# Kernel optimization log

Measured on AMD Instinct MI355X. Metric: run time of the kernel, lower is better.

The kernel has to match this reference:

```python
import jax, jax.numpy as jnp
import numpy as np

FEAT = 64      # feature_dim
HEADS = 4      # n_head
LATENT = 256   # latent_dim
G = 128        # num graphs
NPG = 150      # nodes per graph (<=180 for one-hot positions)
N = G * NPG    # 19200 nodes
E = N * 12     # 230400 edges (excl. self loops)
POS = 180      # one-hot position classes
SLOPE = 0.2    # PyG GATConv leaky_relu negative slope


def gat_conv(x, src, dst, W, att_s, att_d, bias):
    """PyG GATConv (concat heads, self loops already appended to src/dst)."""
    n = x.shape[0]
    h = (x @ W).reshape(n, HEADS, FEAT)                 # [N,H,F]
    a_s = jnp.sum(h * att_s, axis=-1)                   # [N,H]
    a_d = jnp.sum(h * att_d, axis=-1)                   # [N,H]
    e = jax.nn.leaky_relu(a_s[src] + a_d[dst], SLOPE)   # [E,H] per-edge logits
    m = jax.ops.segment_max(e, dst, num_segments=n)     # segment softmax over dst
    ex = jnp.exp(e - m[dst])
    s = jax.ops.segment_sum(ex, dst, num_segments=n)
    alpha = ex / (s[dst] + 1e-16)
    out = jax.ops.segment_sum(h[src] * alpha[:, :, None], dst, num_segments=n)
    return out.reshape(n, HEADS * FEAT) + bias


def setup_inputs() -> dict:
    key = jax.random.key(0)
    ks = jax.random.split(key, 20)

    def p(k, shape, fan_in):
        return jax.random.normal(k, shape, jnp.float32) / np.sqrt(fan_in).astype(np.float32)

    z = jax.random.normal(ks[0], (G, LATENT), jnp.float32)
    src = jax.random.randint(ks[1], (E,), 0, N, jnp.int32)
    dst = (src + jax.random.randint(ks[2], (E,), 1, N, jnp.int32)) % N  # no self loops
    edge_index = jnp.stack([src, dst])
    batch = jnp.repeat(jnp.arange(G, dtype=jnp.int32), NPG)

    in1 = FEAT + POS
    in2 = FEAT * HEADS
    inp = dict(z=z, edge_index=edge_index, batch=batch, num_graphs=G)
    inp.update(
        W0=p(ks[3], (LATENT, FEAT), LATENT), b0=jnp.zeros(FEAT, jnp.float32),
        W1=p(ks[4], (in1, HEADS * FEAT), in1),
        as1=p(ks[5], (HEADS, FEAT), FEAT), ad1=p(ks[6], (HEADS, FEAT), FEAT),
        bb1=jnp.zeros(HEADS * FEAT, jnp.float32),
        W2=p(ks[7], (in2, HEADS * FEAT), in2),
        as2=p(ks[8], (HEADS, FEAT), FEAT), ad2=p(ks[9], (HEADS, FEAT), FEAT),
        bb2=jnp.zeros(HEADS * FEAT, jnp.float32),
        W3=p(ks[10], (in2, HEADS * FEAT), in2),
        as3=p(ks[11], (HEADS, FEAT), FEAT), ad3=p(ks[12], (HEADS, FEAT), FEAT),
        bb3=jnp.zeros(HEADS * FEAT, jnp.float32),
        Wg=p(ks[13], (in2, FEAT), in2), bg=jnp.zeros(FEAT, jnp.float32),
        Wf=p(ks[14], (FEAT, 5), FEAT), bf=jnp.zeros(5, jnp.float32),
    )
    return inp


def reference(z, edge_index, batch, num_graphs,
              W0, b0, W1, as1, ad1, bb1, W2, as2, ad2, bb2,
              W3, as3, ad3, bb3, Wg, bg, Wf, bf):
    n = batch.shape[0]
    x = z @ W0 + b0                                    # dec_feature_init
    x = x[batch]                                       # broadcast graph latent to nodes
    # node_order_within_batch (batch is sorted)
    counts = jax.ops.segment_sum(jnp.ones_like(batch), batch, num_segments=num_graphs)
    starts = jnp.cumsum(counts) - counts
    order = jnp.arange(n, dtype=batch.dtype) - starts[batch]
    pos = jax.nn.one_hot(order, POS, dtype=x.dtype)
    x = jax.nn.relu(jnp.concatenate([x, pos], axis=1))
    # GATConv adds self loops by default
    loops = jnp.arange(n, dtype=edge_index.dtype)
    src = jnp.concatenate([edge_index[0], loops])
    dst = jnp.concatenate([edge_index[1], loops])
    x = jax.nn.relu(gat_conv(x, src, dst, W1, as1, ad1, bb1))
    x = jax.nn.relu(gat_conv(x, src, dst, W2, as2, ad2, bb2))
    x = jax.nn.relu(gat_conv(x, src, dst, W3, as3, ad3, bb3))
    x = jax.nn.relu(x @ Wg + bg)                       # dec_geo
    return x @ Wf + bf                                 # fc_geo -> [N,5]
```

## Files before the change

### kernel.cpp

```cpp
#include <hip/hip_runtime.h>
#include <hip/hip_fp16.h>

#define GNUM 128
#define HEADS 4
#define FEAT 64
#define CH 256
#define LAT 256
#define SLOPE 0.2f
#define CAP 64
#define POSMAX 180

typedef _Float16 h16;
typedef __attribute__((ext_vector_type(4))) _Float16 half4;
typedef __attribute__((ext_vector_type(8))) _Float16 half8;
typedef __attribute__((ext_vector_type(4))) float floatx4;

__device__ __forceinline__ float lrelu(float x) { return fmaxf(x, SLOPE * x); }

__global__ __launch_bounds__(256) void k_setup(const int* __restrict__ batch, int* __restrict__ cnt,
                                               int* __restrict__ starts, int n,
                                               const float* __restrict__ W2, const float* __restrict__ W3,
                                               const float* __restrict__ Wg, h16* __restrict__ W2T,
                                               h16* __restrict__ W3T, h16* __restrict__ WgT,
                                               const float* __restrict__ z, const float* __restrict__ W0,
                                               const float* __restrict__ b0, const float* __restrict__ W1,
                                               const float* __restrict__ as1, const float* __restrict__ ad1,
                                               float* __restrict__ A, float* __restrict__ asg,
                                               float* __restrict__ adg, float* __restrict__ asp,
                                               float* __restrict__ adp) {
  __shared__ float red[4][FEAT];
  __shared__ float xzs[FEAT];
  int bx = blockIdx.x, t = threadIdx.x;
  if (bx < 576) {
    int idx = bx * 256 + t;
    if (idx < n) {
      cnt[idx] = 0;
      int b = batch[idx];
      if (idx == 0 || batch[idx - 1] != b) starts[b] = idx;
    }
    if (idx < 65536) {
      int kb = idx >> 13, rem = idx & 8191, j = rem >> 8, nn = rem & 255;
      W2T[kb * 8192 + nn * 32 + j] = (h16)W2[(kb * 32 + j) * 256 + nn];
    } else if (idx < 131072) {
      int l = idx - 65536;
      int kb = l >> 13, rem = l & 8191, j = rem >> 8, nn = rem & 255;
      W3T[kb * 8192 + nn * 32 + j] = (h16)W3[(kb * 32 + j) * 256 + nn];
    } else {
      int l = idx - 131072;
      int kb = l >> 11, rem = l & 2047, j = rem >> 6, nn = rem & 63;
      WgT[kb * 2048 + nn * 32 + j] = (h16)Wg[(kb * 32 + j) * 64 + nn];
    }
  } else if (bx < 576 + GNUM) {
    int g = bx - 576;
    int f = t & 63, kq = t >> 6;
    float acc = 0.f;
    for (int k = kq * 64; k < kq * 64 + 64; ++k) acc += z[g * LAT + k] * W0[k * FEAT + f];
    red[kq][f] = acc;
    __syncthreads();
    if (kq == 0)
      xzs[f] = fmaxf(red[0][f] + red[1][f] + red[2][f] + red[3][f] + b0[f], 0.f);
    __syncthreads();
    float a2 = 0.f;
#pragma unroll 16
    for (int k = 0; k < FEAT; ++k) a2 += xzs[k] * W1[k * CH + t];
    A[g * CH + t] = a2;
    float ps = a2 * as1[t], pd = a2 * ad1[t];
#pragma unroll
    for (int sh = 1; sh < 64; sh <<= 1) {
      ps += __shfl_xor(ps, sh, 64);
      pd += __shfl_xor(pd, sh, 64);
    }
    if ((t & 63) == 0) {
      asg[g * 4 + (t >> 6)] = ps;
      adg[g * 4 + (t >> 6)] = pd;
    }
  } else {
    int p = bx - (576 + GNUM);
    float wv = W1[(size_t)(FEAT + p) * CH + t];
    float ps = wv * as1[t], pd = wv * ad1[t];
#pragma unroll
    for (int sh = 1; sh < 64; sh <<= 1) {
      ps += __shfl_xor(ps, sh, 64);
      pd += __shfl_xor(pd, sh, 64);
    }
    if ((t & 63) == 0) {
      asp[p * 4 + (t >> 6)] = ps;
      adp[p * 4 + (t >> 6)] = pd;
    }
  }
}

__global__ __launch_bounds__(256) void k_pre(const float* __restrict__ A, const float* __restrict__ W1,
                                             const int* __restrict__ batch, const int* __restrict__ starts,
                                             const float* __restrict__ asg, const float* __restrict__ adg,
                                             const float* __restrict__ asp, const float* __restrict__ adp,
                                             h16* __restrict__ H16, float* __restrict__ a_s,
                                             float* __restrict__ a_d, int n,
                                             const int* __restrict__ src, const int* __restrict__ dst,
                                             int* __restrict__ cnt, int* __restrict__ bucket, int e,
                                             int h1blocks) {
  int t = threadIdx.x;
  if ((int)blockIdx.x < h1blocks) {
    int row = blockIdx.x * 8 + (t >> 5);
    if (row < n) {
      int g = batch[row];
      int p = row - starts[g];
      int c0 = (t & 31) * 8;
      const float* ap = A + g * CH + c0;
      const float* wp = W1 + (size_t)(FEAT + p) * CH + c0;
      float4 a0 = *(const float4*)ap;
      float4 a1 = *(const float4*)(ap + 4);
      float4 w0v = *(const float4*)wp;
      float4 w1v = *(const float4*)(wp + 4);
      half8 o;
      o[0] = (h16)(a0.x + w0v.x); o[1] = (h16)(a0.y + w0v.y);
      o[2] = (h16)(a0.z + w0v.z); o[3] = (h16)(a0.w + w0v.w);
      o[4] = (h16)(a1.x + w1v.x); o[5] = (h16)(a1.y + w1v.y);
      o[6] = (h16)(a1.z + w1v.z); o[7] = (h16)(a1.w + w1v.w);
      *(half8*)(H16 + (size_t)row * CH + c0) = o;
    }
    int idx = blockIdx.x * 256 + t;
    if (idx < n * 4) {
      int nn = idx >> 2, h = idx & 3;
      int g2 = batch[nn], p2 = nn - starts[g2];
      a_s[idx] = asg[g2 * 4 + h] + asp[p2 * 4 + h];
      a_d[idx] = adg[g2 * 4 + h] + adp[p2 * 4 + h];
    }
  } else {
    int i = (blockIdx.x - h1blocks) * 256 + t;
    if (i < e) {
      int d = dst[i];
      int p = atomicAdd(&cnt[d], 1);
      if (p < CAP) bucket[d * CAP + p] = src[i];
    }
  }
}

__global__ __launch_bounds__(1024) void k_fgg(const h16* __restrict__ H16i, const float* __restrict__ a_si,
                                              const float* __restrict__ a_di, const float* __restrict__ bias,
                                              const int* __restrict__ cnt, const int* __restrict__ bucket,
                                              const h16* __restrict__ WT, const float* __restrict__ att_s,
                                              const float* __restrict__ att_d, h16* __restrict__ H16o,
                                              float* __restrict__ a_so, float* __restrict__ a_do_) {
  __shared__ float wsh[16][CAP][4];
  __shared__ int bsh[16][CAP];
  __shared__ __align__(16) h16 Xs[16 * 264];
  __shared__ float pls[16][16];
  __shared__ float pld[16][16];
  int t = threadIdx.x, wv = t >> 6, lane = t & 63;
  int quad = lane >> 4, l15 = lane & 15;
  int row0 = blockIdx.x * 16;
  int n = row0 + wv;
  int hh = lane >> 4, fo = lane * 4;
  {
    int c = min(cnt[n], CAP);
    bool valid = lane < c;
    int sc = valid ? bucket[n * CAP + lane] : n;
    if (valid) bsh[wv][lane] = sc;
    float4 ea4 = *(const float4*)(a_si + (size_t)sc * 4);
    float4 sn4 = *(const float4*)(a_si + (size_t)n * 4);
    float4 dn4 = *(const float4*)(a_di + (size_t)n * 4);
    float ea[4] = {ea4.x, ea4.y, ea4.z, ea4.w};
    float sn[4] = {sn4.x, sn4.y, sn4.z, sn4.w};
    float dn[4] = {dn4.x, dn4.y, dn4.z, dn4.w};
    float asf[4];
#pragma unroll
    for (int h = 0; h < 4; ++h) {
      float e = valid ? lrelu(ea[h] + dn[h]) : -1e30f;
      float es = lrelu(sn[h] + dn[h]);
      float m = e;
#pragma unroll
      for (int sh = 1; sh < 64; sh <<= 1) m = fmaxf(m, __shfl_xor(m, sh, 64));
      m = fmaxf(m, es);
      float wgt = valid ? __expf(e - m) : 0.f;
      float ws = __expf(es - m);
      float s = wgt;
#pragma unroll
      for (int sh = 1; sh < 64; sh <<= 1) s += __shfl_xor(s, sh, 64);
      s += ws;
      float inv = 1.f / (s + 1e-16f);
      if (valid) wsh[wv][lane][h] = wgt * inv;
      asf[h] = ws * inv;
    }
    half4 hv = *(const half4*)(H16i + (size_t)n * CH + fo);
    float a_self = asf[hh];
    float acc0 = a_self * (float)hv[0];
    float acc1 = a_self * (float)hv[1];
    float acc2 = a_self * (float)hv[2];
    float acc3 = a_self * (float)hv[3];
#define GLD(k) (*(const half4*)(H16i + (size_t)bsh[wv][k] * CH + fo))
    half4 q0, q1, q2, q3, q4, q5, q6, q7;
    if (c > 0) q0 = GLD(0);
    if (c > 1) q1 = GLD(1);
    if (c > 2) q2 = GLD(2);
    if (c > 3) q3 = GLD(3);
    if (c > 4) q4 = GLD(4);
    if (c > 5) q5 = GLD(5);
    if (c > 6) q6 = GLD(6);
    if (c > 7) q7 = GLD(7);
    for (int j0 = 0; j0 < c; j0 += 8) {
#define STEP(K, QK)                                              \
      if (j0 + K < c) {                                          \
        float wj = wsh[wv][j0 + K][hh];                          \
        half4 hc = QK;                                           \
        if (j0 + K + 8 < c) QK = GLD(j0 + K + 8);                \
        acc0 += wj * (float)hc[0];                               \
        acc1 += wj * (float)hc[1];                               \
        acc2 += wj * (float)hc[2];                               \
        acc3 += wj * (float)hc[3];                               \
      }
      STEP(0, q0) STEP(1, q1) STEP(2, q2) STEP(3, q3)
      STEP(4, q4) STEP(5, q5) STEP(6, q6) STEP(7, q7)
#undef STEP
    }
#undef GLD
    float4 b4 = *(const float4*)(bias + fo);
    half4 o;
    o[0] = (h16)fmaxf(acc0 + b4.x, 0.f);
    o[1] = (h16)fmaxf(acc1 + b4.y, 0.f);
    o[2] = (h16)fmaxf(acc2 + b4.z, 0.f);
    o[3] = (h16)fmaxf(acc3 + b4.w, 0.f);
    *(half4*)&Xs[wv * 264 + fo] = o;
  }
  __syncthreads();
  floatx4 acc = (floatx4){0.f, 0.f, 0.f, 0.f};
  {
    const h16* bp = WT + (wv * 16 + l15) * 32 + quad * 8;
#pragma unroll
    for (int kb = 0; kb < 8; ++kb) {
      half8 af = *(const half8*)&Xs[l15 * 264 + kb * 32 + quad * 8];
      half8 bf = *(const half8*)(bp + kb * 8192);
      acc = __builtin_amdgcn_mfma_f32_16x16x32_f16(af, bf, acc, 0, 0, 0);
    }
  }
  {
    int col = wv * 16 + l15;
    float asv = att_s[col], adv = att_d[col];
#pragma unroll
    for (int r = 0; r < 4; ++r) {
      float ps = acc[r] * asv;
      float pd = acc[r] * adv;
#pragma unroll
      for (int sh = 1; sh < 16; sh <<= 1) {
        ps += __shfl_xor(ps, sh, 16);
        pd += __shfl_xor(pd, sh, 16);
      }
      if (l15 == 0) {
        pls[quad * 4 + r][wv] = ps;
        pld[quad * 4 + r][wv] = pd;
      }
    }
  }
  __syncthreads();
#pragma unroll
  for (int r = 0; r < 4; ++r)
    Xs[(quad * 4 + r) * 264 + wv * 16 + l15] = (h16)acc[r];
  __syncthreads();
  if (t < 64) {
    int node = t >> 2, head = t & 3;
    a_so[(size_t)(row0 + node) * 4 + head] =
        pls[node][head * 4] + pls[node][head * 4 + 1] + pls[node][head * 4 + 2] + pls[node][head * 4 + 3];
    a_do_[(size_t)(row0 + node) * 4 + head] =
        pld[node][head * 4] + pld[node][head * 4 + 1] + pld[node][head * 4 + 2] + pld[node][head * 4 + 3];
  }
  {
    int row = t >> 6, c4 = (t & 63) * 4;
    *(half4*)(H16o + (size_t)(row0 + row) * CH + c4) = *(const half4*)&Xs[row * 264 + c4];
  }
}

__global__ __launch_bounds__(1024) void k_fgh(const h16* __restrict__ H16i, const float* __restrict__ a_si,
                                              const float* __restrict__ a_di, const float* __restrict__ bias,
                                              const int* __restrict__ cnt, const int* __restrict__ bucket,
                                              const h16* __restrict__ WgT, const float* __restrict__ bg,
                                              const float* __restrict__ Wf, const float* __restrict__ bfv,
                                              float* __restrict__ out) {
  __shared__ float wsh[16][CAP][4];
  __shared__ int bsh[16][CAP];
  __shared__ __align__(16) h16 Xs[16 * 264];
  __shared__ float ytile[16][68];
  __shared__ float WfS[FEAT * 5];
  int t = threadIdx.x, wv = t >> 6, lane = t & 63;
  int quad = lane >> 4, l15 = lane & 15;
  int row0 = blockIdx.x * 16;
  int n = row0 + wv;
  int hh = lane >> 4, fo = lane * 4;
  if (t < FEAT * 5) WfS[t] = Wf[t];
  {
    int c = min(cnt[n], CAP);
    bool valid = lane < c;
    int sc = valid ? bucket[n * CAP + lane] : n;
    if (valid) bsh[wv][lane] = sc;
    float4 ea4 = *(const float4*)(a_si + (size_t)sc * 4);
    float4 sn4 = *(const float4*)(a_si + (size_t)n * 4);
    float4 dn4 = *(const float4*)(a_di + (size_t)n * 4);
    float ea[4] = {ea4.x, ea4.y, ea4.z, ea4.w};
    float sn[4] = {sn4.x, sn4.y, sn4.z, sn4.w};
    float dn[4] = {dn4.x, dn4.y, dn4.z, dn4.w};
    float asf[4];
#pragma unroll
    for (int h = 0; h < 4; ++h) {
      float e = valid ? lrelu(ea[h] + dn[h]) : -1e30f;
      float es = lrelu(sn[h] + dn[h]);
      float m = e;
#pragma unroll
      for (int sh = 1; sh < 64; sh <<= 1) m = fmaxf(m, __shfl_xor(m, sh, 64));
      m = fmaxf(m, es);
      float wgt = valid ? __expf(e - m) : 0.f;
      float ws = __expf(es - m);
      float s = wgt;
#pragma unroll
      for (int sh = 1; sh < 64; sh <<= 1) s += __shfl_xor(s, sh, 64);
      s += ws;
      float inv = 1.f / (s + 1e-16f);
      if (valid) wsh[wv][lane][h] = wgt * inv;
      asf[h] = ws * inv;
    }
    half4 hv = *(const half4*)(H16i + (size_t)n * CH + fo);
    float a_self = asf[hh];
    float acc0 = a_self * (float)hv[0];
    float acc1 = a_self * (float)hv[1];
    float acc2 = a_self * (float)hv[2];
    float acc3 = a_self * (float)hv[3];
#define GLD(k) (*(const half4*)(H16i + (size_t)bsh[wv][k] * CH + fo))
    half4 q0, q1, q2, q3, q4, q5, q6, q7;
    if (c > 0) q0 = GLD(0);
    if (c > 1) q1 = GLD(1);
    if (c > 2) q2 = GLD(2);
    if (c > 3) q3 = GLD(3);
    if (c > 4) q4 = GLD(4);
    if (c > 5) q5 = GLD(5);
    if (c > 6) q6 = GLD(6);
    if (c > 7) q7 = GLD(7);
    for (int j0 = 0; j0 < c; j0 += 8) {
#define STEP(K, QK)                                              \
      if (j0 + K < c) {                                          \
        float wj = wsh[wv][j0 + K][hh];                          \
        half4 hc = QK;                                           \
        if (j0 + K + 8 < c) QK = GLD(j0 + K + 8);                \
        acc0 += wj * (float)hc[0];                               \
        acc1 += wj * (float)hc[1];                               \
        acc2 += wj * (float)hc[2];                               \
        acc3 += wj * (float)hc[3];                               \
      }
      STEP(0, q0) STEP(1, q1) STEP(2, q2) STEP(3, q3)
      STEP(4, q4) STEP(5, q5) STEP(6, q6) STEP(7, q7)
#undef STEP
    }
#undef GLD
    float4 b4 = *(const float4*)(bias + fo);
    half4 o;
    o[0] = (h16)fmaxf(acc0 + b4.x, 0.f);
    o[1] = (h16)fmaxf(acc1 + b4.y, 0.f);
    o[2] = (h16)fmaxf(acc2 + b4.z, 0.f);
    o[3] = (h16)fmaxf(acc3 + b4.w, 0.f);
    *(half4*)&Xs[wv * 264 + fo] = o;
  }
  __syncthreads();
  floatx4 acc = (floatx4){0.f, 0.f, 0.f, 0.f};
  if (wv < 4) {
    const h16* bp = WgT + (wv * 16 + l15) * 32 + quad * 8;
#pragma unroll
    for (int kb = 0; kb < 8; ++kb) {
      half8 af = *(const half8*)&Xs[l15 * 264 + kb * 32 + quad * 8];
      half8 bf = *(const half8*)(bp + kb * 2048);
      acc = __builtin_amdgcn_mfma_f32_16x16x32_f16(af, bf, acc, 0, 0, 0);
    }
  }
  __syncthreads();
  if (wv < 4) {
    int col = wv * 16 + l15;
    float bgv = bg[col];
#pragma unroll
    for (int r = 0; r < 4; ++r)
      ytile[quad * 4 + r][col] = fmaxf(acc[r] + bgv, 0.f);
  }
  __syncthreads();
  if (t < 16 * 5) {
    int row = t / 5, o = t % 5;
    float s = bfv[o];
#pragma unroll
    for (int k = 0; k < FEAT; ++k) s += ytile[row][k] * WfS[k * 5 + o];
    out[(size_t)(row0 + row) * 5 + o] = s;
  }
}

static inline size_t alignup(size_t x) { return (x + 255) & ~(size_t)255; }

extern "C" void kernel_launch(void* const* d_in, const int* in_sizes, int n_in,
                              void* d_out, int out_size, void* d_ws, size_t ws_size,
                              hipStream_t stream) {
  (void)n_in; (void)out_size; (void)ws_size;
  const float* z   = (const float*)d_in[0];
  const int* edge  = (const int*)d_in[1];
  const int* batch = (const int*)d_in[2];
  const float* W0  = (const float*)d_in[4];
  const float* b0  = (const float*)d_in[5];
  const float* W1  = (const float*)d_in[6];
  const float* as1 = (const float*)d_in[7];
  const float* ad1 = (const float*)d_in[8];
  const float* bb1 = (const float*)d_in[9];
  const float* W2  = (const float*)d_in[10];
  const float* as2 = (const float*)d_in[11];
  const float* ad2 = (const float*)d_in[12];
  const float* bb2 = (const float*)d_in[13];
  const float* W3  = (const float*)d_in[14];
  const float* as3 = (const float*)d_in[15];
  const float* ad3 = (const float*)d_in[16];
  const float* bb3 = (const float*)d_in[17];
  const float* Wg  = (const float*)d_in[18];
  const float* bg  = (const float*)d_in[19];
  const float* Wf  = (const float*)d_in[20];
  const float* bfv = (const float*)d_in[21];
  float* out = (float*)d_out;

  const int E = in_sizes[1] / 2;
  const int N = in_sizes[2];
  const int* srcI = edge;
  const int* dstI = edge + E;

  char* w = (char*)d_ws;
  auto carve = [&](size_t bytes) { void* p = (void*)w; w += alignup(bytes); return p; };
  int* starts  = (int*)carve((size_t)GNUM * 4);
  int* cnt     = (int*)carve((size_t)N * 4);
  int* bucket  = (int*)carve((size_t)N * CAP * 4);
  float* A     = (float*)carve((size_t)GNUM * CH * 4);
  float* a_sA  = (float*)carve((size_t)N * 4 * 4);
  float* a_dA  = (float*)carve((size_t)N * 4 * 4);
  float* a_sB  = (float*)carve((size_t)N * 4 * 4);
  float* a_dB  = (float*)carve((size_t)N * 4 * 4);
  float* asg   = (float*)carve((size_t)GNUM * 4 * 4);
  float* adg   = (float*)carve((size_t)GNUM * 4 * 4);
  float* asp   = (float*)carve((size_t)POSMAX * 4 * 4);
  float* adp   = (float*)carve((size_t)POSMAX * 4 * 4);
  h16* W2T     = (h16*)carve((size_t)CH * CH * 2);
  h16* W3T     = (h16*)carve((size_t)CH * CH * 2);
  h16* WgT     = (h16*)carve((size_t)CH * FEAT * 2);
  h16* H16a    = (h16*)carve((size_t)N * CH * 2);
  h16* H16b    = (h16*)carve((size_t)N * CH * 2);

  int h1blocks = N / 8;
  int ebl = (E + 255) / 256;

  hipLaunchKernelGGL(k_setup, dim3(576 + GNUM + POSMAX), dim3(256), 0, stream,
                     batch, cnt, starts, N, W2, W3, Wg, W2T, W3T, WgT, z, W0, b0, W1,
                     as1, ad1, A, asg, adg, asp, adp);
  hipLaunchKernelGGL(k_pre, dim3(h1blocks + ebl), dim3(256), 0, stream,
                     A, W1, batch, starts, asg, adg, asp, adp, H16a, a_sA, a_dA, N,
                     srcI, dstI, cnt, bucket, E, h1blocks);
  hipLaunchKernelGGL(k_fgg, dim3(N / 16), dim3(1024), 0, stream,
                     H16a, a_sA, a_dA, bb1, cnt, bucket, W2T, as2, ad2, H16b, a_sB, a_dB);
  hipLaunchKernelGGL(k_fgg, dim3(N / 16), dim3(1024), 0, stream,
                     H16b, a_sB, a_dB, bb2, cnt, bucket, W3T, as3, ad3, H16a, a_sA, a_dA);
  hipLaunchKernelGGL(k_fgh, dim3(N / 16), dim3(1024), 0, stream,
                     H16a, a_sA, a_dA, bb3, cnt, bucket, WgT, bg, Wf, bfv, out);
}
```

Measured before the change: 265.3 us.

## Process 64 nodes per block in fused GAT kernels to raise weight reuse

Each 1024-thread block now aggregates 64 nodes (4 per wave, sequentially) instead of 16, then runs a 64x256 MFMA tile where each wave computes four 16x16 output tiles sharing one A fragment. This amortizes global loads of the transposed weight matrix over four times more rows and removes the shared-memory partial reduction for attention logits by writing per-head sums directly. Shared memory is reorganized into a single buffer with aliasing. The trade-off is fewer blocks (300), a serial aggregation loop per wave, higher register use for four accumulators, and larger LDS footprint, which may reduce occupancy and latency hiding for the gather phase.

```diff
diff --git a/kernel.cpp b/kernel.cpp
--- a/kernel.cpp
+++ b/kernel.cpp
@@ -142,21 +142,20 @@
                                               const h16* __restrict__ WT, const float* __restrict__ att_s,
                                               const float* __restrict__ att_d, h16* __restrict__ H16o,
                                               float* __restrict__ a_so, float* __restrict__ a_do_) {
-  __shared__ float wsh[16][CAP][4];
-  __shared__ int bsh[16][CAP];
-  __shared__ __align__(16) h16 Xs[16 * 264];
-  __shared__ float pls[16][16];
-  __shared__ float pld[16][16];
+  __shared__ __align__(16) char smemc[54272];
+  h16* Xs = (h16*)smemc;
+  float* wsh = (float*)(smemc + 33792);
+  int* bsh = (int*)(smemc + 50176);
   int t = threadIdx.x, wv = t >> 6, lane = t & 63;
   int quad = lane >> 4, l15 = lane & 15;
-  int row0 = blockIdx.x * 16;
-  int n = row0 + wv;
+  int row0 = blockIdx.x * 64;
   int hh = lane >> 4, fo = lane * 4;
-  {
+  for (int i = 0; i < 4; ++i) {
+    int n = row0 + wv * 4 + i;
     int c = min(cnt[n], CAP);
     bool valid = lane < c;
     int sc = valid ? bucket[n * CAP + lane] : n;
-    if (valid) bsh[wv][lane] = sc;
+    if (valid) bsh[wv * CAP + lane] = sc;
     float4 ea4 = *(const float4*)(a_si + (size_t)sc * 4);
     float4 sn4 = *(const float4*)(a_si + (size_t)n * 4);
     float4 dn4 = *(const float4*)(a_di + (size_t)n * 4);
@@ -179,7 +178,7 @@
       for (int sh = 1; sh < 64; sh <<= 1) s += __shfl_xor(s, sh, 64);
       s += ws;
       float inv = 1.f / (s + 1e-16f);
-      if (valid) wsh[wv][lane][h] = wgt * inv;
+      if (valid) wsh[(wv * CAP + lane) * 4 + h] = wgt * inv;
       asf[h] = ws * inv;
     }
     half4 hv = *(const half4*)(H16i + (size_t)n * CH + fo);
@@ -188,7 +187,7 @@
     float acc1 = a_self * (float)hv[1];
     float acc2 = a_self * (float)hv[2];
     float acc3 = a_self * (float)hv[3];
-#define GLD(k) (*(const half4*)(H16i + (size_t)bsh[wv][k] * CH + fo))
+#define GLD(k) (*(const half4*)(H16i + (size_t)bsh[wv * CAP + (k)] * CH + fo))
     half4 q0, q1, q2, q3, q4, q5, q6, q7;
     if (c > 0) q0 = GLD(0);
     if (c > 1) q1 = GLD(1);
@@ -201,7 +200,7 @@
     for (int j0 = 0; j0 < c; j0 += 8) {
 #define STEP(K, QK)                                              \
       if (j0 + K < c) {                                          \
-        float wj = wsh[wv][j0 + K][hh];                          \
+        float wj = wsh[(wv * CAP + j0 + K) * 4 + hh];            \
         half4 hc = QK;                                           \
         if (j0 + K + 8 < c) QK = GLD(j0 + K + 8);                \
         acc0 += wj * (float)hc[0];                               \
@@ -220,52 +219,64 @@
     o[1] = (h16)fmaxf(acc1 + b4.y, 0.f);
     o[2] = (h16)fmaxf(acc2 + b4.z, 0.f);
     o[3] = (h16)fmaxf(acc3 + b4.w, 0.f);
-    *(half4*)&Xs[wv * 264 + fo] = o;
+    *(half4*)&Xs[(wv * 4 + i) * 264 + fo] = o;
   }
   __syncthreads();
-  floatx4 acc = (floatx4){0.f, 0.f, 0.f, 0.f};
+  int rb = wv >> 2, cs = wv & 3;
+  floatx4 acc[4];
+#pragma unroll
+  for (int nt = 0; nt < 4; ++nt) acc[nt] = (floatx4){0.f, 0.f, 0.f, 0.f};
+#pragma unroll
+  for (int kb = 0; kb < 8; ++kb) {
+    half8 af = *(const half8*)&Xs[(rb * 16 + l15) * 264 + kb * 32 + quad * 8];
+    const h16* bp = WT + kb * 8192 + (cs * 64 + l15) * 32 + quad * 8;
+    half8 b0 = *(const half8*)(bp + 0 * 512);
+    half8 b1 = *(const half8*)(bp + 1 * 512);
+    half8 b2 = *(const half8*)(bp + 2 * 512);
+    half8 b3 = *(const half8*)(bp + 3 * 512);
+    acc[0] = __builtin_amdgcn_mfma_f32_16x16x32_f16(af, b0, acc[0], 0, 0, 0);
+    acc[1] = __builtin_amdgcn_mfma_f32_16x16x32_f16(af, b1, acc[1], 0, 0, 0);
+    acc[2] = __builtin_amdgcn_mfma_f32_16x16x32_f16(af, b2, acc[2], 0, 0, 0);
+    acc[3] = __builtin_amdgcn_mfma_f32_16x16x32_f16(af, b3, acc[3], 0, 0, 0);
+  }
   {
-    const h16* bp = WT + (wv * 16 + l15) * 32 + quad * 8;
-#pragma unroll
-    for (int kb = 0; kb < 8; ++kb) {
-      half8 af = *(const half8*)&Xs[l15 * 264 + kb * 32 + quad * 8];
-      half8 bf = *(const half8*)(bp + kb * 8192);
-      acc = __builtin_amdgcn_mfma_f32_16x16x32_f16(af, bf, acc, 0, 0, 0);
-    }
-  }
-  {
-    int col = wv * 16 + l15;
-    float asv = att_s[col], adv = att_d[col];
+    float asv[4], adv[4];
+#pragma unroll
+    for (int nt = 0; nt < 4; ++nt) {
+      asv[nt] = att_s[cs * FEAT + nt * 16 + l15];
+      adv[nt] = att_d[cs * FEAT + nt * 16 + l15];
+    }
 #pragma unroll
     for (int r = 0; r < 4; ++r) {
-      float ps = acc[r] * asv;
-      float pd = acc[r] * adv;
+      float ps = acc[0][r] * asv[0] + acc[1][r] * asv[1] +
+                 acc[2][r] * asv[2] + acc[3][r] * asv[3];
+      float pd = acc[0][r] * adv[0] + acc[1][r] * adv[1] +
+                 acc[2][r] * adv[2] + acc[3][r] * adv[3];
 #pragma unroll
       for (int sh = 1; sh < 16; sh <<= 1) {
         ps += __shfl_xor(ps, sh, 16);
         pd += __shfl_xor(pd, sh, 16);
       }
       if (l15 == 0) {
-        pls[quad * 4 + r][wv] = ps;
-        pld[quad * 4 + r][wv] = pd;
+        int row = row0 + rb * 16 + quad * 4 + r;
+        a_so[(size_t)row * 4 + cs] = ps;
+        a_do_[(size_t)row * 4 + cs] = pd;
       }
     }
   }
   __syncthreads();
 #pragma unroll
-  for (int r = 0; r < 4; ++r)
-    Xs[(quad * 4 + r) * 264 + wv * 16 + l15] = (h16)acc[r];
+  for (int nt = 0; nt < 4; ++nt)
+#pragma unroll
+    for (int r = 0; r < 4; ++r)
+      Xs[(rb * 16 + quad * 4 + r) * 264 + cs * 64 + nt * 16 + l15] = (h16)acc[nt][r];
   __syncthreads();
-  if (t < 64) {
-    int node = t >> 2, head = t & 3;
-    a_so[(size_t)(row0 + node) * 4 + head] =
-        pls[node][head * 4] + pls[node][head * 4 + 1] + pls[node][head * 4 + 2] + pls[node][head * 4 + 3];
-    a_do_[(size_t)(row0 + node) * 4 + head] =
-        pld[node][head * 4] + pld[node][head * 4 + 1] + pld[node][head * 4 + 2] + pld[node][head * 4 + 3];
-  }
   {
-    int row = t >> 6, c4 = (t & 63) * 4;
-    *(half4*)(H16o + (size_t)(row0 + row) * CH + c4) = *(const half4*)&Xs[row * 264 + c4];
+    int row = t >> 4, seg = t & 15;
+    const h16* srcr = &Xs[row * 264 + seg * 16];
+    h16* dstr = H16o + (size_t)(row0 + row) * CH + seg * 16;
+    *(half8*)(dstr + 0) = *(const half8*)(srcr + 0);
+    *(half8*)(dstr + 8) = *(const half8*)(srcr + 8);
   }
 }
 
@@ -275,22 +286,22 @@
                                               const h16* __restrict__ WgT, const float* __restrict__ bg,
                                               const float* __restrict__ Wf, const float* __restrict__ bfv,
                                               float* __restrict__ out) {
-  __shared__ float wsh[16][CAP][4];
-  __shared__ int bsh[16][CAP];
-  __shared__ __align__(16) h16 Xs[16 * 264];
-  __shared__ float ytile[16][68];
-  __shared__ float WfS[FEAT * 5];
+  __shared__ __align__(16) char smemc[55552];
+  h16* Xs = (h16*)smemc;
+  float* wsh = (float*)(smemc + 33792);
+  int* bsh = (int*)(smemc + 50176);
+  float* WfS = (float*)(smemc + 54272);
   int t = threadIdx.x, wv = t >> 6, lane = t & 63;
   int quad = lane >> 4, l15 = lane & 15;
-  int row0 = blockIdx.x * 16;
-  int n = row0 + wv;
+  int row0 = blockIdx.x * 64;
   int hh = lane >> 4, fo = lane * 4;
   if (t < FEAT * 5) WfS[t] = Wf[t];
-  {
+  for (int i = 0; i < 4; ++i) {
+    int n = row0 + wv * 4 + i;
     int c = min(cnt[n], CAP);
     bool valid = lane < c;
     int sc = valid ? bucket[n * CAP + lane] : n;
-    if (valid) bsh[wv][lane] = sc;
+    if (valid) bsh[wv * CAP + lane] = sc;
     float4 ea4 = *(const float4*)(a_si + (size_t)sc * 4);
     float4 sn4 = *(const float4*)(a_si + (size_t)n * 4);
     float4 dn4 = *(const float4*)(a_di + (size_t)n * 4);
@@ -313,7 +324,7 @@
       for (int sh = 1; sh < 64; sh <<= 1) s += __shfl_xor(s, sh, 64);
       s += ws;
       float inv = 1.f / (s + 1e-16f);
-      if (valid) wsh[wv][lane][h] = wgt * inv;
+      if (valid) wsh[(wv * CAP + lane) * 4 + h] = wgt * inv;
       asf[h] = ws * inv;
     }
     half4 hv = *(const half4*)(H16i + (size_t)n * CH + fo);
@@ -322,7 +333,7 @@
     float acc1 = a_self * (float)hv[1];
     float acc2 = a_self * (float)hv[2];
     float acc3 = a_self * (float)hv[3];
-#define GLD(k) (*(const half4*)(H16i + (size_t)bsh[wv][k] * CH + fo))
+#define GLD(k) (*(const half4*)(H16i + (size_t)bsh[wv * CAP + (k)] * CH + fo))
     half4 q0, q1, q2, q3, q4, q5, q6, q7;
     if (c > 0) q0 = GLD(0);
     if (c > 1) q1 = GLD(1);
@@ -335,7 +346,7 @@
     for (int j0 = 0; j0 < c; j0 += 8) {
 #define STEP(K, QK)                                              \
       if (j0 + K < c) {                                          \
-        float wj = wsh[wv][j0 + K][hh];                          \
+        float wj = wsh[(wv * CAP + j0 + K) * 4 + hh];            \
         half4 hc = QK;                                           \
         if (j0 + K + 8 < c) QK = GLD(j0 + K + 8);                \
         acc0 += wj * (float)hc[0];                               \
@@ -354,33 +365,31 @@
     o[1] = (h16)fmaxf(acc1 + b4.y, 0.f);
     o[2] = (h16)fmaxf(acc2 + b4.z, 0.f);
     o[3] = (h16)fmaxf(acc3 + b4.w, 0.f);
-    *(half4*)&Xs[wv * 264 + fo] = o;
+    *(half4*)&Xs[(wv * 4 + i) * 264 + fo] = o;
   }
   __syncthreads();
+  int rb = wv >> 2, cs = wv & 3;
   floatx4 acc = (floatx4){0.f, 0.f, 0.f, 0.f};
-  if (wv < 4) {
-    const h16* bp = WgT + (wv * 16 + l15) * 32 + quad * 8;
-#pragma unroll
-    for (int kb = 0; kb < 8; ++kb) {
-      half8 af = *(const half8*)&Xs[l15 * 264 + kb * 32 + quad * 8];
-      half8 bf = *(const half8*)(bp + kb * 2048);
-      acc = __builtin_amdgcn_mfma_f32_16x16x32_f16(af, bf, acc, 0, 0, 0);
-    }
+#pragma unroll
+  for (int kb = 0; kb < 8; ++kb) {
+    half8 af = *(const half8*)&Xs[(rb * 16 + l15) * 264 + kb * 32 + quad * 8];
+    half8 bf = *(const half8*)(WgT + kb * 2048 + (cs * 16 + l15) * 32 + quad * 8);
+    acc = __builtin_amdgcn_mfma_f32_16x16x32_f16(af, bf, acc, 0, 0, 0);
+  }
+  float* ytile = (float*)(smemc + 33792);
+  {
+    int col = cs * 16 + l15;
+    float bgv = bg[col];
+#pragma unroll
+    for (int r = 0; r < 4; ++r)
+      ytile[(rb * 16 + quad * 4 + r) * 68 + col] = fmaxf(acc[r] + bgv, 0.f);
   }
   __syncthreads();
-  if (wv < 4) {
-    int col = wv * 16 + l15;
-    float bgv = bg[col];
-#pragma unroll
-    for (int r = 0; r < 4; ++r)
-      ytile[quad * 4 + r][col] = fmaxf(acc[r] + bgv, 0.f);
-  }
-  __syncthreads();
-  if (t < 16 * 5) {
+  if (t < 64 * 5) {
     int row = t / 5, o = t % 5;
     float s = bfv[o];
 #pragma unroll
-    for (int k = 0; k < FEAT; ++k) s += ytile[row][k] * WfS[k * 5 + o];
+    for (int k = 0; k < FEAT; ++k) s += ytile[row * 68 + k] * WfS[k * 5 + o];
     out[(size_t)(row0 + row) * 5 + o] = s;
   }
 }
@@ -448,10 +457,10 @@
   hipLaunchKernelGGL(k_pre, dim3(h1blocks + ebl), dim3(256), 0, stream,
                      A, W1, batch, starts, asg, adg, asp, adp, H16a, a_sA, a_dA, N,
                      srcI, dstI, cnt, bucket, E, h1blocks);
-  hipLaunchKernelGGL(k_fgg, dim3(N / 16), dim3(1024), 0, stream,
+  hipLaunchKernelGGL(k_fgg, dim3(N / 64), dim3(1024), 0, stream,
                      H16a, a_sA, a_dA, bb1, cnt, bucket, W2T, as2, ad2, H16b, a_sB, a_dB);
-  hipLaunchKernelGGL(k_fgg, dim3(N / 16), dim3(1024), 0, stream,
+  hipLaunchKernelGGL(k_fgg, dim3(N / 64), dim3(1024), 0, stream,
                      H16b, a_sB, a_dB, bb2, cnt, bucket, W3T, as3, ad3, H16a, a_sA, a_dA);
-  hipLaunchKernelGGL(k_fgh, dim3(N / 16), dim3(1024), 0, stream,
+  hipLaunchKernelGGL(k_fgh, dim3(N / 64), dim3(1024), 0, stream,
                      H16a, a_sA, a_dA, bb3, cnt, bucket, WgT, bg, Wf, bfv, out);
 }
```

Result: slower. 336.2 us (+26.7%).

## Halve fused GAT block to 512 threads, two nodes per wave

Applied to the files above, without the earlier changes.

The fused aggregation+GEMM kernels now launch 512 threads (8 waves) per 16-node tile instead of 1024. Each wave aggregates two destination nodes in sequence and computes two 16-column MFMA tiles, so each A-fragment load from LDS is reused twice. Shared scratch shrinks, one barrier is removed from the epilogue, and the global store is widened to half8. Per-wave neighbor aggregation becomes serial over two nodes, which adds latency per block in exchange for better occupancy and fewer barriers.

```diff
diff --git a/kernel.cpp b/kernel.cpp
--- a/kernel.cpp
+++ b/kernel.cpp
@@ -136,23 +136,23 @@
   }
 }
 
-__global__ __launch_bounds__(1024) void k_fgg(const h16* __restrict__ H16i, const float* __restrict__ a_si,
-                                              const float* __restrict__ a_di, const float* __restrict__ bias,
-                                              const int* __restrict__ cnt, const int* __restrict__ bucket,
-                                              const h16* __restrict__ WT, const float* __restrict__ att_s,
-                                              const float* __restrict__ att_d, h16* __restrict__ H16o,
-                                              float* __restrict__ a_so, float* __restrict__ a_do_) {
-  __shared__ float wsh[16][CAP][4];
-  __shared__ int bsh[16][CAP];
+__global__ __launch_bounds__(512) void k_fgg(const h16* __restrict__ H16i, const float* __restrict__ a_si,
+                                             const float* __restrict__ a_di, const float* __restrict__ bias,
+                                             const int* __restrict__ cnt, const int* __restrict__ bucket,
+                                             const h16* __restrict__ WT, const float* __restrict__ att_s,
+                                             const float* __restrict__ att_d, h16* __restrict__ H16o,
+                                             float* __restrict__ a_so, float* __restrict__ a_do_) {
   __shared__ __align__(16) h16 Xs[16 * 264];
-  __shared__ float pls[16][16];
-  __shared__ float pld[16][16];
+  __shared__ float wsh[8][CAP][4];
+  __shared__ int bsh[8][CAP];
+  __shared__ float pls[16][8];
+  __shared__ float pld[16][8];
   int t = threadIdx.x, wv = t >> 6, lane = t & 63;
   int quad = lane >> 4, l15 = lane & 15;
   int row0 = blockIdx.x * 16;
-  int n = row0 + wv;
   int hh = lane >> 4, fo = lane * 4;
-  {
+  for (int i = 0; i < 2; ++i) {
+    int n = row0 + wv * 2 + i;
     int c = min(cnt[n], CAP);
     bool valid = lane < c;
     int sc = valid ? bucket[n * CAP + lane] : n;
@@ -220,26 +220,32 @@
     o[1] = (h16)fmaxf(acc1 + b4.y, 0.f);
     o[2] = (h16)fmaxf(acc2 + b4.z, 0.f);
     o[3] = (h16)fmaxf(acc3 + b4.w, 0.f);
-    *(half4*)&Xs[wv * 264 + fo] = o;
+    *(half4*)&Xs[(wv * 2 + i) * 264 + fo] = o;
   }
   __syncthreads();
-  floatx4 acc = (floatx4){0.f, 0.f, 0.f, 0.f};
+  floatx4 acc[2];
+  acc[0] = (floatx4){0.f, 0.f, 0.f, 0.f};
+  acc[1] = acc[0];
+#pragma unroll
+  for (int kb = 0; kb < 8; ++kb) {
+    half8 af = *(const half8*)&Xs[l15 * 264 + kb * 32 + quad * 8];
+    const h16* bp = WT + kb * 8192 + (wv * 32 + l15) * 32 + quad * 8;
+    half8 b0 = *(const half8*)(bp + 0);
+    half8 b1 = *(const half8*)(bp + 512);
+    acc[0] = __builtin_amdgcn_mfma_f32_16x16x32_f16(af, b0, acc[0], 0, 0, 0);
+    acc[1] = __builtin_amdgcn_mfma_f32_16x16x32_f16(af, b1, acc[1], 0, 0, 0);
+  }
   {
-    const h16* bp = WT + (wv * 16 + l15) * 32 + quad * 8;
-#pragma unroll
-    for (int kb = 0; kb < 8; ++kb) {
-      half8 af = *(const half8*)&Xs[l15 * 264 + kb * 32 + quad * 8];
-      half8 bf = *(const half8*)(bp + kb * 8192);
-      acc = __builtin_amdgcn_mfma_f32_16x16x32_f16(af, bf, acc, 0, 0, 0);
-    }
-  }
-  {
-    int col = wv * 16 + l15;
-    float asv = att_s[col], adv = att_d[col];
+    float asv[2], adv[2];
+#pragma unroll
+    for (int nt = 0; nt < 2; ++nt) {
+      asv[nt] = att_s[wv * 32 + nt * 16 + l15];
+      adv[nt] = att_d[wv * 32 + nt * 16 + l15];
+    }
 #pragma unroll
     for (int r = 0; r < 4; ++r) {
-      float ps = acc[r] * asv;
-      float pd = acc[r] * adv;
+      float ps = acc[0][r] * asv[0] + acc[1][r] * asv[1];
+      float pd = acc[0][r] * adv[0] + acc[1][r] * adv[1];
 #pragma unroll
       for (int sh = 1; sh < 16; sh <<= 1) {
         ps += __shfl_xor(ps, sh, 16);
@@ -253,40 +259,41 @@
   }
   __syncthreads();
 #pragma unroll
-  for (int r = 0; r < 4; ++r)
-    Xs[(quad * 4 + r) * 264 + wv * 16 + l15] = (h16)acc[r];
-  __syncthreads();
+  for (int nt = 0; nt < 2; ++nt)
+#pragma unroll
+    for (int r = 0; r < 4; ++r)
+      Xs[(quad * 4 + r) * 264 + wv * 32 + nt * 16 + l15] = (h16)acc[nt][r];
   if (t < 64) {
     int node = t >> 2, head = t & 3;
-    a_so[(size_t)(row0 + node) * 4 + head] =
-        pls[node][head * 4] + pls[node][head * 4 + 1] + pls[node][head * 4 + 2] + pls[node][head * 4 + 3];
-    a_do_[(size_t)(row0 + node) * 4 + head] =
-        pld[node][head * 4] + pld[node][head * 4 + 1] + pld[node][head * 4 + 2] + pld[node][head * 4 + 3];
-  }
+    a_so[(size_t)(row0 + node) * 4 + head] = pls[node][head * 2] + pls[node][head * 2 + 1];
+    a_do_[(size_t)(row0 + node) * 4 + head] = pld[node][head * 2] + pld[node][head * 2 + 1];
+  }
+  __syncthreads();
   {
-    int row = t >> 6, c4 = (t & 63) * 4;
-    *(half4*)(H16o + (size_t)(row0 + row) * CH + c4) = *(const half4*)&Xs[row * 264 + c4];
+    int row = t >> 5, seg = t & 31;
+    *(half8*)(H16o + (size_t)(row0 + row) * CH + seg * 8) =
+        *(const half8*)&Xs[row * 264 + seg * 8];
   }
 }
 
-__global__ __launch_bounds__(1024) void k_fgh(const h16* __restrict__ H16i, const float* __restrict__ a_si,
-                                              const float* __restrict__ a_di, const float* __restrict__ bias,
-                                              const int* __restrict__ cnt, const int* __restrict__ bucket,
-                                              const h16* __restrict__ WgT, const float* __restrict__ bg,
-                                              const float* __restrict__ Wf, const float* __restrict__ bfv,
-                                              float* __restrict__ out) {
-  __shared__ float wsh[16][CAP][4];
-  __shared__ int bsh[16][CAP];
+__global__ __launch_bounds__(512) void k_fgh(const h16* __restrict__ H16i, const float* __restrict__ a_si,
+                                             const float* __restrict__ a_di, const float* __restrict__ bias,
+                                             const int* __restrict__ cnt, const int* __restrict__ bucket,
+                                             const h16* __restrict__ WgT, const float* __restrict__ bg,
+                                             const float* __restrict__ Wf, const float* __restrict__ bfv,
+                                             float* __restrict__ out) {
   __shared__ __align__(16) h16 Xs[16 * 264];
+  __shared__ float wsh[8][CAP][4];
+  __shared__ int bsh[8][CAP];
   __shared__ float ytile[16][68];
   __shared__ float WfS[FEAT * 5];
   int t = threadIdx.x, wv = t >> 6, lane = t & 63;
   int quad = lane >> 4, l15 = lane & 15;
   int row0 = blockIdx.x * 16;
-  int n = row0 + wv;
   int hh = lane >> 4, fo = lane * 4;
   if (t < FEAT * 5) WfS[t] = Wf[t];
-  {
+  for (int i = 0; i < 2; ++i) {
+    int n = row0 + wv * 2 + i;
     int c = min(cnt[n], CAP);
     bool valid = lane < c;
     int sc = valid ? bucket[n * CAP + lane] : n;
@@ -354,21 +361,17 @@
     o[1] = (h16)fmaxf(acc1 + b4.y, 0.f);
     o[2] = (h16)fmaxf(acc2 + b4.z, 0.f);
     o[3] = (h16)fmaxf(acc3 + b4.w, 0.f);
-    *(half4*)&Xs[wv * 264 + fo] = o;
+    *(half4*)&Xs[(wv * 2 + i) * 264 + fo] = o;
   }
   __syncthreads();
-  floatx4 acc = (floatx4){0.f, 0.f, 0.f, 0.f};
   if (wv < 4) {
-    const h16* bp = WgT + (wv * 16 + l15) * 32 + quad * 8;
+    floatx4 acc = (floatx4){0.f, 0.f, 0.f, 0.f};
 #pragma unroll
     for (int kb = 0; kb < 8; ++kb) {
       half8 af = *(const half8*)&Xs[l15 * 264 + kb * 32 + quad * 8];
-      half8 bf = *(const half8*)(bp + kb * 2048);
+      half8 bf = *(const half8*)(WgT + kb * 2048 + (wv * 16 + l15) * 32 + quad * 8);
       acc = __builtin_amdgcn_mfma_f32_16x16x32_f16(af, bf, acc, 0, 0, 0);
     }
-  }
-  __syncthreads();
-  if (wv < 4) {
     int col = wv * 16 + l15;
     float bgv = bg[col];
 #pragma unroll
@@ -448,10 +451,10 @@
   hipLaunchKernelGGL(k_pre, dim3(h1blocks + ebl), dim3(256), 0, stream,
                      A, W1, batch, starts, asg, adg, asp, adp, H16a, a_sA, a_dA, N,
                      srcI, dstI, cnt, bucket, E, h1blocks);
-  hipLaunchKernelGGL(k_fgg, dim3(N / 16), dim3(1024), 0, stream,
+  hipLaunchKernelGGL(k_fgg, dim3(N / 16), dim3(512), 0, stream,
                      H16a, a_sA, a_dA, bb1, cnt, bucket, W2T, as2, ad2, H16b, a_sB, a_dB);
-  hipLaunchKernelGGL(k_fgg, dim3(N / 16), dim3(1024), 0, stream,
+  hipLaunchKernelGGL(k_fgg, dim3(N / 16), dim3(512), 0, stream,
                      H16b, a_sB, a_dB, bb2, cnt, bucket, W3T, as3, ad3, H16a, a_sA, a_dA);
-  hipLaunchKernelGGL(k_fgh, dim3(N / 16), dim3(1024), 0, stream,
+  hipLaunchKernelGGL(k_fgh, dim3(N / 16), dim3(512), 0, stream,
                      H16a, a_sA, a_dA, bb3, cnt, bucket, WgT, bg, Wf, bfv, out);
 }
```

Result: no change. 267.0 us (+0.6%).
